# Optimization experiments

Measured on AMD Instinct MI355X. Metric: run time of the kernel, lower is better.

The kernel has to match this reference:

```python
import jax, jax.numpy as jnp
import numpy as np

N = 100000      # nodes
E = 1600000     # edges
G = 64          # graphs in batch
H = 128         # hidden (== num_features)
L = 4           # num_layers
C = 16          # num_classes
NCAND = 100000  # candidate edges
BN_EPS = 1e-5


def setup_inputs() -> dict:
    key = jax.random.key(0)
    ks = jax.random.split(key, 24)
    s = 0.05
    inp = {}
    inp["x"] = jax.random.normal(ks[0], (N, H), dtype=jnp.float32)
    inp["edge_index"] = jax.random.randint(ks[1], (2, E), 0, N)
    inp["batch"] = jnp.sort(jax.random.randint(ks[2], (N,), 0, G))
    inp["candidate_edges"] = jax.random.randint(ks[3], (2, NCAND), 0, N)
    # GIN conv params, stacked over L layers (all layers are H->H since num_features==hidden)
    inp["cW1"] = jax.random.normal(ks[4], (L, H, H), dtype=jnp.float32) * s
    inp["cb1"] = jnp.zeros((L, H), jnp.float32)
    inp["cW2"] = jax.random.normal(ks[5], (L, H, H), dtype=jnp.float32) * s
    inp["cb2"] = jnp.zeros((L, H), jnp.float32)
    inp["cgamma"] = jnp.ones((L, H), jnp.float32)
    inp["cbeta"] = jnp.zeros((L, H), jnp.float32)
    inp["ceps"] = jnp.zeros((L,), jnp.float32)  # train_eps=True, init 0
    # node classifier: L*H -> 2H -> H -> H -> C (dropout is identity in eval)
    inp["ncW1"] = jax.random.normal(ks[6], (L * H, 2 * H), dtype=jnp.float32) * s
    inp["ncb1"] = jnp.zeros((2 * H,), jnp.float32)
    inp["ncW2"] = jax.random.normal(ks[7], (2 * H, H), dtype=jnp.float32) * s
    inp["ncb2"] = jnp.zeros((H,), jnp.float32)
    inp["ncW3"] = jax.random.normal(ks[8], (H, H), dtype=jnp.float32) * s
    inp["ncb3"] = jnp.zeros((H,), jnp.float32)
    inp["ncW4"] = jax.random.normal(ks[9], (H, C), dtype=jnp.float32) * s
    inp["ncb4"] = jnp.zeros((C,), jnp.float32)
    # edge predictor: 2*L*H -> 2H -> H -> 1
    inp["epW1"] = jax.random.normal(ks[10], (2 * L * H, 2 * H), dtype=jnp.float32) * s
    inp["epb1"] = jnp.zeros((2 * H,), jnp.float32)
    inp["epW2"] = jax.random.normal(ks[11], (2 * H, H), dtype=jnp.float32) * s
    inp["epb2"] = jnp.zeros((H,), jnp.float32)
    inp["epW3"] = jax.random.normal(ks[12], (H, 1), dtype=jnp.float32) * s
    inp["epb3"] = jnp.zeros((1,), jnp.float32)
    return inp


def _forward(x, cW1, cb1, cW2, cb2, cgamma, cbeta, ceps,
             ncW1, ncb1, ncW2, ncb2, ncW3, ncb3, ncW4, ncb4,
             epW1, epb1, epW2, epb2, epW3, epb3,
             edge_index, batch, candidate_edges):
    src, dst = edge_index[0], edge_index[1]
    h = x
    xs = []
    for l in range(L):
        # GIN: (1+eps)*x_i + sum_{j->i} x_j  (scatter-add over destination nodes)
        agg = jax.ops.segment_sum(h[src], dst, num_segments=N)
        z = (1.0 + ceps[l]) * h + agg
        z = jax.nn.relu(z @ cW1[l] + cb1[l])
        z = jax.nn.relu(z @ cW2[l] + cb2[l])
        # BatchNorm1d (training-mode batch statistics, biased variance)
        mu = z.mean(axis=0)
        var = jnp.var(z, axis=0)
        h = (z - mu) * jax.lax.rsqrt(var + BN_EPS) * cgamma[l] + cbeta[l]
        xs.append(h)
    emb = jnp.concatenate(xs, axis=-1)  # [N, L*H]
    # global mean pool over graphs
    sums = jax.ops.segment_sum(emb, batch, num_segments=G)
    cnt = jax.ops.segment_sum(jnp.ones((N, 1), emb.dtype), batch, num_segments=G)
    gemb = sums / jnp.maximum(cnt, 1.0)  # [G, L*H]
    t = jax.nn.relu(gemb @ ncW1 + ncb1)
    t = jax.nn.relu(t @ ncW2 + ncb2)
    t = jax.nn.relu(t @ ncW3 + ncb3)
    class_output = jax.nn.log_softmax(t @ ncW4 + ncb4, axis=1)  # [G, C]
    # link prediction: gather node embeddings per candidate edge
    ef = jnp.concatenate([emb[candidate_edges[0]], emb[candidate_edges[1]]], axis=1)  # [NC, 2*L*H]
    u = jax.nn.relu(ef @ epW1 + epb1)
    u = jax.nn.relu(u @ epW2 + epb2)
    edge_scores = jax.nn.sigmoid((u @ epW3 + epb3).squeeze(-1))  # [NC]
    return class_output, edge_scores


def reference(x, cW1, cb1, cW2, cb2, cgamma, cbeta, ceps,
              ncW1, ncb1, ncW2, ncb2, ncW3, ncb3, ncW4, ncb4,
              epW1, epb1, epW2, epb2, epW3, epb3,
              edge_index, batch, candidate_edges):
    return _forward(x, cW1, cb1, cW2, cb2, cgamma, cbeta, ceps,
                    ncW1, ncb1, ncW2, ncb2, ncW3, ncb3, ncW4, ncb4,
                    epW1, epb1, epW2, epb2, epW3, epb3,
                    edge_index, batch, candidate_edges)
```

## Files before the change

kernel.cpp:

```cpp
#include <hip/hip_runtime.h>
#include <math.h>

#define NN 100000
#define EE 1600000
#define GG 64
#define HH 128
#define LL 4
#define CCLS 16
#define NC 100000
#define NB 49
#define LDK 40
#define LDA2 136
#define LDC 260

typedef __attribute__((ext_vector_type(8))) short bf16x8;
typedef __attribute__((ext_vector_type(4))) float f32x4;

__device__ __forceinline__ unsigned short f2bf(float x) {
  union { float f; unsigned int u; } v; v.f = x;
  unsigned int r = v.u + 0x7fffu + ((v.u >> 16) & 1u);
  return (unsigned short)(r >> 16);
}
__device__ __forceinline__ float bl(unsigned u) {
  union { unsigned u; float f; } v; v.u = u << 16; return v.f;
}
__device__ __forceinline__ float bh(unsigned u) {
  union { unsigned u; float f; } v; v.u = u & 0xffff0000u; return v.f;
}

__global__ void hist_kernel(const int* __restrict__ dst, int* __restrict__ cnt, int E) {
  int e = blockIdx.x * 256 + threadIdx.x;
  if (e < E) atomicAdd(&cnt[dst[e]], 1);
}

__global__ __launch_bounds__(256) void scan_p1(const int* __restrict__ cnt,
                                               int* __restrict__ bsum, int n) {
  __shared__ int red[256];
  int tid = threadIdx.x;
  int base = blockIdx.x * 1024 + tid * 4;
  int s = 0;
  if (base + 3 < n) {
    int4 v = *(const int4*)(cnt + base);
    s = v.x + v.y + v.z + v.w;
  } else {
    for (int i = 0; i < 4; ++i) if (base + i < n) s += cnt[base + i];
  }
  red[tid] = s;
  __syncthreads();
  for (int st = 128; st >= 1; st >>= 1) {
    if (tid < st) red[tid] += red[tid + st];
    __syncthreads();
  }
  if (tid == 0) bsum[blockIdx.x] = red[0];
}

__global__ void scan_p2(int* __restrict__ bsum, int* __restrict__ rowptr,
                        int* __restrict__ bcursor, int nb, int n) {
  __shared__ int buf[128];
  int tid = threadIdx.x;
  int v = (tid < nb) ? bsum[tid] : 0;
  buf[tid] = v;
  __syncthreads();
  for (int off = 1; off < 128; off <<= 1) {
    int t = (tid >= off) ? buf[tid - off] : 0;
    __syncthreads();
    buf[tid] += t;
    __syncthreads();
  }
  if (tid < nb) bsum[tid] = buf[tid] - v;
  if (tid == 127) rowptr[n] = buf[127];
  __syncthreads();
  if (tid < NB) bcursor[tid] = bsum[2 * tid];
}

__global__ __launch_bounds__(256) void scan_p3(const int* __restrict__ cnt,
                                               const int* __restrict__ bsum,
                                               int* __restrict__ rowptr,
                                               int* __restrict__ cursor, int n) {
  __shared__ int red[256];
  int tid = threadIdx.x;
  int base = blockIdx.x * 1024 + tid * 4;
  int v[4] = {0, 0, 0, 0};
  if (base + 3 < n) {
    int4 t = *(const int4*)(cnt + base);
    v[0] = t.x; v[1] = t.y; v[2] = t.z; v[3] = t.w;
  } else {
    for (int i = 0; i < 4; ++i) if (base + i < n) v[i] = cnt[base + i];
  }
  int s = v[0] + v[1] + v[2] + v[3];
  red[tid] = s;
  __syncthreads();
  for (int off = 1; off < 256; off <<= 1) {
    int t = (tid >= off) ? red[tid - off] : 0;
    __syncthreads();
    red[tid] += t;
    __syncthreads();
  }
  int run = bsum[blockIdx.x] + red[tid] - s;
  int4 o;
  o.x = run; o.y = run + v[0]; o.z = o.y + v[1]; o.w = o.z + v[2];
  if (base + 3 < n) {
    *(int4*)(rowptr + base) = o;
    *(int4*)(cursor + base) = o;
  } else {
    int oo[4] = {o.x, o.y, o.z, o.w};
    for (int i = 0; i < 4; ++i)
      if (base + i < n) { rowptr[base + i] = oo[i]; cursor[base + i] = oo[i]; }
  }
}

__global__ __launch_bounds__(256) void partition_kernel(const int* __restrict__ src,
                                                        const int* __restrict__ dst,
                                                        int* __restrict__ bcursor,
                                                        int2* __restrict__ pairs, int E) {
  __shared__ int sS[4096];
  __shared__ int sD[4096];
  __shared__ int hist[NB];
  __shared__ int base[NB];
  int tid = threadIdx.x;
  int base_e = blockIdx.x * 4096;
  int cnt = min(4096, E - base_e);
  if (tid < NB) hist[tid] = 0;
  for (int i = tid * 4; i < cnt; i += 1024) {
    if (i + 3 < cnt) {
      *(int4*)(sS + i) = *(const int4*)(src + base_e + i);
      *(int4*)(sD + i) = *(const int4*)(dst + base_e + i);
    } else {
      for (int k = i; k < cnt; ++k) { sS[k] = src[base_e + k]; sD[k] = dst[base_e + k]; }
    }
  }
  __syncthreads();
  for (int i = tid; i < cnt; i += 256) atomicAdd(&hist[sD[i] >> 11], 1);
  __syncthreads();
  if (tid < NB) {
    base[tid] = atomicAdd(&bcursor[tid], hist[tid]);
    hist[tid] = 0;
  }
  __syncthreads();
  for (int i = tid; i < cnt; i += 256) {
    int d = sD[i];
    int b = d >> 11;
    int off = atomicAdd(&hist[b], 1);
    pairs[base[b] + off] = make_int2(sS[i], d);
  }
}

__global__ __launch_bounds__(256) void scatter_csr(const int2* __restrict__ pairs,
                                                   const int* __restrict__ rowptr,
                                                   int* __restrict__ cursor,
                                                   int* __restrict__ csr_src) {
  int b = blockIdx.x % 56;
  int slice = blockIdx.x / 56;
  if (b >= NB) return;
  int start = rowptr[b * 2048];
  int endn = min((b + 1) * 2048, NN);
  int end = rowptr[endn];
  for (int i = start + slice * 256 + threadIdx.x; i < end; i += 8 * 256) {
    int2 p = pairs[i];
    int pos = atomicAdd(&cursor[p.y], 1);
    csr_src[pos] = p.x;
  }
}

#define NF2B (NN * HH / 4)
#define NCVW (LL * 16384 + 262144 + 32768)
__global__ void convert_all(const float* __restrict__ x, unsigned short* __restrict__ x16,
                            const float* __restrict__ cW1, const float* __restrict__ cW2,
                            unsigned short* __restrict__ WT1, unsigned short* __restrict__ WT2,
                            const float* __restrict__ epW1, unsigned short* __restrict__ W1T,
                            const float* __restrict__ epW2, unsigned short* __restrict__ W2T) {
  int gi = blockIdx.x * 256 + threadIdx.x;
  if (gi < NF2B) {
    float4 v = ((const float4*)x)[gi];
    unsigned short r[4] = {f2bf(v.x), f2bf(v.y), f2bf(v.z), f2bf(v.w)};
    *(uint2*)(x16 + (size_t)gi * 4) = *(uint2*)r;
    return;
  }
  int idx = gi - NF2B;
  if (idx < LL * 16384) {
    int l = idx >> 14, r = idx & 16383, k = r >> 7, n = r & 127;
    WT1[l * 16384 + n * 128 + k] = f2bf(cW1[idx]);
    WT2[l * 16384 + n * 128 + k] = f2bf(cW2[idx]);
  } else if (idx < LL * 16384 + 262144) {
    int j = idx - LL * 16384;
    int k = j >> 8, n = j & 255;
    W1T[(size_t)n * 1024 + k] = f2bf(epW1[j]);
  } else if (idx < NCVW) {
    int j = idx - LL * 16384 - 262144;
    int k = j >> 7, n = j & 127;
    W2T[(size_t)n * 256 + k] = f2bf(epW2[j]);
  }
}

__global__ void aggregate_bf16(const unsigned short* __restrict__ h16, int ld,
                               const int* __restrict__ rowptr,
                               const int* __restrict__ csr_src,
                               const float* __restrict__ ceps_l,
                               const float* __restrict__ bnsum_prev,
                               const float* __restrict__ bnsumsq_prev,
                               const float* __restrict__ gamma_prev,
                               const float* __restrict__ beta_prev,
                               unsigned short* __restrict__ out, int n) {
  int wave = threadIdx.x >> 6;
  int lane = threadIdx.x & 63;
  int sub = lane >> 4;
  int li = lane & 15;
  int node = blockIdx.x * 16 + wave * 4 + sub;
  if (node >= n) return;
  int c8 = li * 8;
  float eps1 = 1.0f + *ceps_l;
  float sc[8], off[8];
  if (bnsum_prev) {
    const float inv_n = 1.0f / (float)NN;
#pragma unroll
    for (int k = 0; k < 8; ++k) {
      int c = c8 + k;
      float mu = bnsum_prev[c] * inv_n;
      float var = bnsumsq_prev[c] * inv_n - mu * mu;
      float s = rsqrtf(var + 1e-5f) * gamma_prev[c];
      sc[k] = s;
      off[k] = beta_prev[c] - s * mu;
    }
  } else {
#pragma unroll
    for (int k = 0; k < 8; ++k) { sc[k] = 1.f; off[k] = 0.f; }
  }
  float acc[8] = {};
  int b = rowptr[node], e = rowptr[node + 1];
  int j = b;
  for (; j + 8 <= e; j += 8) {
    uint4 u[8];
#pragma unroll
    for (int t = 0; t < 8; ++t) {
      int s = csr_src[j + t];
      u[t] = *(const uint4*)(h16 + (size_t)s * ld + c8);
    }
#pragma unroll
    for (int t = 0; t < 8; ++t) {
      acc[0] += bl(u[t].x); acc[1] += bh(u[t].x);
      acc[2] += bl(u[t].y); acc[3] += bh(u[t].y);
      acc[4] += bl(u[t].z); acc[5] += bh(u[t].z);
      acc[6] += bl(u[t].w); acc[7] += bh(u[t].w);
    }
  }
  for (; j < e; ++j) {
    int s = csr_src[j];
    uint4 u = *(const uint4*)(h16 + (size_t)s * ld + c8);
    acc[0] += bl(u.x); acc[1] += bh(u.x);
    acc[2] += bl(u.y); acc[3] += bh(u.y);
    acc[4] += bl(u.z); acc[5] += bh(u.z);
    acc[6] += bl(u.w); acc[7] += bh(u.w);
  }
  uint4 hu = *(const uint4*)(h16 + (size_t)node * ld + c8);
  acc[0] = fmaf(eps1, bl(hu.x), acc[0]); acc[1] = fmaf(eps1, bh(hu.x), acc[1]);
  acc[2] = fmaf(eps1, bl(hu.y), acc[2]); acc[3] = fmaf(eps1, bh(hu.y), acc[3]);
  acc[4] = fmaf(eps1, bl(hu.z), acc[4]); acc[5] = fmaf(eps1, bh(hu.z), acc[5]);
  acc[6] = fmaf(eps1, bl(hu.w), acc[6]); acc[7] = fmaf(eps1, bh(hu.w), acc[7]);
  float degw = (float)(e - b) + eps1;
  unsigned short o[8];
#pragma unroll
  for (int i = 0; i < 8; ++i) o[i] = f2bf(fmaf(sc[i], acc[i], degw * off[i]));
  *(uint4*)(out + (size_t)node * 128 + c8) = *(uint4*)o;
}

__global__ __launch_bounds__(256) void trunk_fused(
    const unsigned short* __restrict__ A16,
    const unsigned short* __restrict__ W1T, const float* __restrict__ b1,
    const unsigned short* __restrict__ W2T, const float* __restrict__ b2,
    float* __restrict__ bnsum, float* __restrict__ bnsumsq,
    unsigned short* __restrict__ C16 , int M) {
  __shared__ unsigned short As[128 * LDA2];
  __shared__ unsigned short Bs[128 * LDA2];
  const int tid = threadIdx.x;
  const int bm = blockIdx.x * 128;
  const int lane = tid & 63;
  const int wave = tid >> 6;
  const int wr = (wave >> 1) << 6;
  const int wc = (wave & 1) << 6;
  const int ar = tid >> 1;
  const int ah = (tid & 1) << 4;
  int gra = bm + ar; if (gra >= M) gra = M - 1;
  const unsigned short* Arow = A16 + (size_t)gra * 128;
  const unsigned short* B1row = W1T + (size_t)ar * 128;
  const int mrow = lane & 15;
  const int kq = (lane >> 4) << 3;

  {
    uint4 aR[8], bR[8];
#pragma unroll
    for (int i = 0; i < 4; ++i) {
      aR[2 * i]     = *(const uint4*)(Arow + (i << 5) + ah);
      aR[2 * i + 1] = *(const uint4*)(Arow + (i << 5) + ah + 8);
      bR[2 * i]     = *(const uint4*)(B1row + (i << 5) + ah);
      bR[2 * i + 1] = *(const uint4*)(B1row + (i << 5) + ah + 8);
    }
#pragma unroll
    for (int i = 0; i < 4; ++i) {
      *(uint4*)(As + ar * LDA2 + (i << 5) + ah)     = aR[2 * i];
      *(uint4*)(As + ar * LDA2 + (i << 5) + ah + 8) = aR[2 * i + 1];
      *(uint4*)(Bs + ar * LDA2 + (i << 5) + ah)     = bR[2 * i];
      *(uint4*)(Bs + ar * LDA2 + (i << 5) + ah + 8) = bR[2 * i + 1];
    }
  }
  f32x4 acc[4][4] = {};
  __syncthreads();
#pragma unroll
  for (int ks = 0; ks < 4; ++ks) {
    const int k0 = ks << 5;
    bf16x8 af[4], bfv[4];
#pragma unroll
    for (int t = 0; t < 4; ++t)
      af[t] = *(const bf16x8*)(As + (wr + t * 16 + mrow) * LDA2 + k0 + kq);
#pragma unroll
    for (int t = 0; t < 4; ++t)
      bfv[t] = *(const bf16x8*)(Bs + (wc + t * 16 + mrow) * LDA2 + k0 + kq);
#pragma unroll
    for (int mt = 0; mt < 4; ++mt)
#pragma unroll
      for (int nt = 0; nt < 4; ++nt)
        acc[mt][nt] = __builtin_amdgcn_mfma_f32_16x16x32_bf16(af[mt], bfv[nt], acc[mt][nt], 0, 0, 0);
  }
  uint4 w2[8];
  {
    const unsigned short* B2row = W2T + (size_t)ar * 128;
#pragma unroll
    for (int i = 0; i < 4; ++i) {
      w2[2 * i]     = *(const uint4*)(B2row + (i << 5) + ah);
      w2[2 * i + 1] = *(const uint4*)(B2row + (i << 5) + ah + 8);
    }
  }
  __syncthreads();
  const int crow = (lane >> 4) << 2;
  const int ccol = lane & 15;
#pragma unroll
  for (int nt = 0; nt < 4; ++nt) {
    int c = wc + nt * 16 + ccol;
    float bz = b1[c];
#pragma unroll
    for (int mt = 0; mt < 4; ++mt) {
      int rl = wr + mt * 16 + crow;
#pragma unroll
      for (int i = 0; i < 4; ++i)
        As[(rl + i) * LDA2 + c] = f2bf(fmaxf(acc[mt][nt][i] + bz, 0.f));
    }
  }
#pragma unroll
  for (int i = 0; i < 4; ++i) {
    *(uint4*)(Bs + ar * LDA2 + (i << 5) + ah)     = w2[2 * i];
    *(uint4*)(Bs + ar * LDA2 + (i << 5) + ah + 8) = w2[2 * i + 1];
  }
#pragma unroll
  for (int mt = 0; mt < 4; ++mt)
#pragma unroll
    for (int nt = 0; nt < 4; ++nt)
      acc[mt][nt] = (f32x4){0.f, 0.f, 0.f, 0.f};
  __syncthreads();
#pragma unroll
  for (int ks = 0; ks < 4; ++ks) {
    const int k0 = ks << 5;
    bf16x8 af[4], bfv[4];
#pragma unroll
    for (int t = 0; t < 4; ++t)
      af[t] = *(const bf16x8*)(As + (wr + t * 16 + mrow) * LDA2 + k0 + kq);
#pragma unroll
    for (int t = 0; t < 4; ++t)
      bfv[t] = *(const bf16x8*)(Bs + (wc + t * 16 + mrow) * LDA2 + k0 + kq);
#pragma unroll
    for (int mt = 0; mt < 4; ++mt)
#pragma unroll
      for (int nt = 0; nt < 4; ++nt)
        acc[mt][nt] = __builtin_amdgcn_mfma_f32_16x16x32_bf16(af[mt], bfv[nt], acc[mt][nt], 0, 0, 0);
  }
  __syncthreads();
#pragma unroll
  for (int nt = 0; nt < 4; ++nt) {
    int c = wc + nt * 16 + ccol;
    float bz = b2[c];
    float s = 0.f, q = 0.f;
#pragma unroll
    for (int mt = 0; mt < 4; ++mt) {
      int rl = wr + mt * 16 + crow;
      int rbase = bm + rl;
#pragma unroll
      for (int i = 0; i < 4; ++i) {
        float v = fmaxf(acc[mt][nt][i] + bz, 0.f);
        Bs[(rl + i) * LDA2 + c] = f2bf(v);
        if (rbase + i < M) { s += v; q += v * v; }
      }
    }
    s += __shfl_xor(s, 16, 64);
    s += __shfl_xor(s, 32, 64);
    q += __shfl_xor(q, 16, 64);
    q += __shfl_xor(q, 32, 64);
    if (lane < 16) {
      atomicAdd(&bnsum[c], s);
      atomicAdd(&bnsumsq[c], q);
    }
  }
  __syncthreads();
#pragma unroll
  for (int p = 0; p < 8; ++p) {
    int r = p * 16 + (tid >> 4);
    int q8 = (tid & 15) * 8;
    if (bm + r < M)
      *(uint4*)(C16 + (size_t)(bm + r) * 512 + q8) =
          *(const uint4*)(Bs + r * LDA2 + q8);
  }
}

__global__ void bn_all(unsigned short* __restrict__ z ,
                       const float* __restrict__ sum, const float* __restrict__ sumsq,
                       const float* __restrict__ gamma, const float* __restrict__ beta) {
  int idx = blockIdx.x * 256 + threadIdx.x;
  if (idx >= NN * 64) return;
  int r = idx >> 6, c8 = (idx & 63) << 3;
  uint4 v = *(const uint4*)(z + (size_t)r * 512 + c8);
  float f[8] = {bl(v.x), bh(v.x), bl(v.y), bh(v.y), bl(v.z), bh(v.z), bl(v.w), bh(v.w)};
  const float inv_n = 1.0f / (float)NN;
  unsigned short o[8];
#pragma unroll
  for (int j = 0; j < 8; ++j) {
    int c = c8 + j;
    float mu = sum[c] * inv_n;
    float var = sumsq[c] * inv_n - mu * mu;
    float scv = rsqrtf(var + 1e-5f) * gamma[c];
    o[j] = f2bf((f[j] - mu) * scv + beta[c]);
  }
  *(uint4*)(z + (size_t)r * 512 + c8) = *(uint4*)o;
}

__global__ __launch_bounds__(512, 4) void ep_fused(
    const unsigned short* __restrict__ emb16, const int* __restrict__ cand,
    const unsigned short* __restrict__ W1T ,
    const float* __restrict__ b1,
    const unsigned short* __restrict__ W2T ,
    const float* __restrict__ b2, const float* __restrict__ epW3,
    const float* __restrict__ epb3,
    float* __restrict__ out, int M) {
  __shared__ unsigned short smem[128 * LDC];
  __shared__ float sDotA[128];
  __shared__ float sDotB[128];
  unsigned short* const As0 = smem;
  unsigned short* const As1 = smem + 128 * LDK;
  unsigned short* const Bs0 = smem + 2 * 128 * LDK;
  unsigned short* const Bs1 = smem + 2 * 128 * LDK + 256 * LDK;
  const int tid = threadIdx.x;
  const int bm = blockIdx.x * 128;
  const int lane = tid & 63;
  const int wave = tid >> 6;
  const int wr = (wave >> 2) << 6;
  const int wc = (wave & 3) << 6;
  f32x4 acc[4][4] = {};
  const int ar = tid >> 2;
  const int ah = (tid & 3) << 3;
  int gra = bm + ar; if (gra >= M) gra = M - 1;
  const int node0 = cand[gra];
  const int node1 = cand[NC + gra];
  const int br = tid >> 1;
  const int bh8 = (tid & 1) << 4;
  const unsigned short* Brow = W1T + (size_t)br * 1024 + bh8;
  const unsigned short* Arow0 = emb16 + (size_t)node0 * 512 + ah;
  const unsigned short* Arow1 = emb16 + (size_t)node1 * 512 + ah - 512;
  const int mrow = lane & 15;
  const int kq = (lane >> 4) << 3;

  auto ldA = [&](int k) -> uint4 {
    const unsigned short* p = (k < 16) ? Arow0 : Arow1;
    return *(const uint4*)(p + (k << 5));
  };
  auto ldB0v = [&](int k) -> uint4 { return *(const uint4*)(Brow + (k << 5)); };
  auto ldB1v = [&](int k) -> uint4 { return *(const uint4*)(Brow + (k << 5) + 8); };
  auto stTile = [&](unsigned short* Ab, unsigned short* Bb, uint4 a, uint4 x0, uint4 x1) {
    *(uint4*)(Ab + ar * LDK + ah) = a;
    *(uint4*)(Bb + br * LDK + bh8) = x0;
    *(uint4*)(Bb + br * LDK + bh8 + 8) = x1;
  };
  auto mma_step = [&](const unsigned short* A, const unsigned short* B) {
    bf16x8 af[4], bfv[4];
#pragma unroll
    for (int t = 0; t < 4; ++t)
      af[t] = *(const bf16x8*)(A + (wr + t * 16 + mrow) * LDK + kq);
#pragma unroll
    for (int t = 0; t < 4; ++t)
      bfv[t] = *(const bf16x8*)(B + (wc + t * 16 + mrow) * LDK + kq);
#pragma unroll
    for (int mt = 0; mt < 4; ++mt)
#pragma unroll
      for (int nt = 0; nt < 4; ++nt)
        acc[mt][nt] = __builtin_amdgcn_mfma_f32_16x16x32_bf16(af[mt], bfv[nt], acc[mt][nt], 0, 0, 0);
  };

  uint4 aA, aB, b0, b1v;
  {
    uint4 a0 = ldA(0), x0 = ldB0v(0), x1 = ldB1v(0);
    stTile(As0, Bs0, a0, x0, x1);
    aA = ldA(1); b0 = ldB0v(1); b1v = ldB1v(1);
    aB = ldA(2);
  }
  __syncthreads();
  for (int it = 0; it < 16; ++it) {
    const int s0 = 2 * it;
    stTile(As1, Bs1, aA, b0, b1v);
    if (s0 + 3 < 32) aA = ldA(s0 + 3);
    if (s0 + 2 < 32) { b0 = ldB0v(s0 + 2); b1v = ldB1v(s0 + 2); }
    mma_step(As0, Bs0);
    __syncthreads();
    const int s1 = s0 + 1;
    if (s1 < 31) {
      stTile(As0, Bs0, aB, b0, b1v);
      if (s1 + 3 < 32) aB = ldA(s1 + 3);
      if (s1 + 2 < 32) { b0 = ldB0v(s1 + 2); b1v = ldB1v(s1 + 2); }
    }
    mma_step(As1, Bs1);
    __syncthreads();
  }

  const int crow = (lane >> 4) << 2;
  const int ccol = lane & 15;
#pragma unroll
  for (int nt = 0; nt < 4; ++nt) {
    int c = wc + nt * 16 + ccol;
    float bz = b1[c];
#pragma unroll
    for (int mt = 0; mt < 4; ++mt) {
      int rl = wr + mt * 16 + crow;
#pragma unroll
      for (int i = 0; i < 4; ++i)
        smem[(rl + i) * LDC + c] = f2bf(fmaxf(acc[mt][nt][i] + bz, 0.f));
    }
  }
  __syncthreads();
  const int wr2 = (wave >> 1) << 5;
  const int wc2 = (wave & 1) << 6;
  f32x4 acc2[2][4] = {};
  for (int ks = 0; ks < 8; ++ks) {
    const int k0 = ks << 5;
    bf16x8 af[2], bfv[4];
#pragma unroll
    for (int t = 0; t < 2; ++t)
      af[t] = *(const bf16x8*)(smem + (wr2 + t * 16 + mrow) * LDC + k0 + kq);
#pragma unroll
    for (int t = 0; t < 4; ++t)
      bfv[t] = *(const bf16x8*)(W2T + (size_t)(wc2 + t * 16 + mrow) * 256 + k0 + kq);
#pragma unroll
    for (int mt = 0; mt < 2; ++mt)
#pragma unroll
      for (int nt = 0; nt < 4; ++nt)
        acc2[mt][nt] = __builtin_amdgcn_mfma_f32_16x16x32_bf16(af[mt], bfv[nt], acc2[mt][nt], 0, 0, 0);
  }
  float w3v[4], bz2[4];
#pragma unroll
  for (int nt = 0; nt < 4; ++nt) {
    int c = wc2 + nt * 16 + ccol;
    w3v[nt] = epW3[c];
    bz2[nt] = b2[c];
  }
  float* sBank = (wave & 1) ? sDotB : sDotA;
#pragma unroll
  for (int mt = 0; mt < 2; ++mt) {
#pragma unroll
    for (int i = 0; i < 4; ++i) {
      int rl = wr2 + mt * 16 + crow + i;
      float p = 0.f;
#pragma unroll
      for (int nt = 0; nt < 4; ++nt)
        p = fmaf(fmaxf(acc2[mt][nt][i] + bz2[nt], 0.f), w3v[nt], p);
      p += __shfl_xor(p, 1, 64);
      p += __shfl_xor(p, 2, 64);
      p += __shfl_xor(p, 4, 64);
      p += __shfl_xor(p, 8, 64);
      if ((lane & 15) == 0) sBank[rl] = p;
    }
  }
  __syncthreads();
  if (tid < 128) {
    int r = bm + tid;
    if (r < M) out[r] = 1.f / (1.f + expf(-(sDotA[tid] + sDotB[tid] + epb3[0])));
  }
}

__global__ __launch_bounds__(256) void pool_bf16(const unsigned short* __restrict__ emb16,
                                                 const int* __restrict__ batch,
                                                 float* __restrict__ gsum) {
  __shared__ int se[2];
  __shared__ float sRed[512];
  int g = blockIdx.x;
  int chunk = blockIdx.y;
  int tid = threadIdx.x;
  if (tid < 2) {
    int x = g + tid;
    int lo = 0, hi = NN;
    while (lo < hi) {
      int mid = (lo + hi) >> 1;
      if (batch[mid] < x) lo = mid + 1; else hi = mid;
    }
    se[tid] = lo;
  }
  __syncthreads();
  int s = se[0], e = se[1];
  int len = e - s;
  int per = (len + 7) >> 3;
  int r0 = s + chunk * per;
  int r1 = min(r0 + per, e);
  int c8 = (tid & 63) * 8;
  int wgrp = tid >> 6;
  float acc[8] = {};
  for (int r = r0 + wgrp; r < r1; r += 4) {
    uint4 u = *(const uint4*)(emb16 + (size_t)r * 512 + c8);
    acc[0] += bl(u.x); acc[1] += bh(u.x);
    acc[2] += bl(u.y); acc[3] += bh(u.y);
    acc[4] += bl(u.z); acc[5] += bh(u.z);
    acc[6] += bl(u.w); acc[7] += bh(u.w);
  }
  if (wgrp == 0) {
#pragma unroll
    for (int j = 0; j < 8; ++j) sRed[c8 + j] = acc[j];
  }
  __syncthreads();
  for (int w = 1; w < 4; ++w) {
    if (wgrp == w) {
#pragma unroll
      for (int j = 0; j < 8; ++j) sRed[c8 + j] += acc[j];
    }
    __syncthreads();
  }
  if (r0 < r1 && tid < 128) {
#pragma unroll
    for (int j = 0; j < 4; ++j)
      atomicAdd(&gsum[g * 512 + tid * 4 + j], sRed[tid * 4 + j]);
  }
}

__global__ __launch_bounds__(256) void nc_fused(
    const float* __restrict__ gsum, const int* __restrict__ batch,
    const float* __restrict__ W1, const float* __restrict__ b1,
    const float* __restrict__ W2, const float* __restrict__ b2,
    const float* __restrict__ W3, const float* __restrict__ b3,
    const float* __restrict__ W4, const float* __restrict__ b4,
    float* __restrict__ out) {
  __shared__ float row[512];
  __shared__ float t1[256];
  __shared__ float t2[128];
  __shared__ float t3s[128];
  __shared__ float lg[16];
  __shared__ int se[2];
  int g = blockIdx.x;
  int tid = threadIdx.x;
  if (tid < 2) {
    int x = g + tid;
    int lo = 0, hi = NN;
    while (lo < hi) {
      int mid = (lo + hi) >> 1;
      if (batch[mid] < x) lo = mid + 1; else hi = mid;
    }
    se[tid] = lo;
  }
  __syncthreads();
  float inv = 1.0f / fmaxf((float)(se[1] - se[0]), 1.0f);
  row[tid] = gsum[g * 512 + tid] * inv;
  row[tid + 256] = gsum[g * 512 + tid + 256] * inv;
  __syncthreads();
  {
    float acc = b1[tid];
#pragma unroll 8
    for (int k = 0; k < 512; ++k) acc = fmaf(row[k], W1[k * 256 + tid], acc);
    t1[tid] = fmaxf(acc, 0.f);
  }
  __syncthreads();
  if (tid < 128) {
    float acc = b2[tid];
#pragma unroll 8
    for (int k = 0; k < 256; ++k) acc = fmaf(t1[k], W2[k * 128 + tid], acc);
    t2[tid] = fmaxf(acc, 0.f);
  }
  __syncthreads();
  if (tid < 128) {
    float acc = b3[tid];
#pragma unroll 8
    for (int k = 0; k < 128; ++k) acc = fmaf(t2[k], W3[k * 128 + tid], acc);
    t3s[tid] = fmaxf(acc, 0.f);
  }
  __syncthreads();
  if (tid < 16) {
    float acc = b4[tid];
#pragma unroll 8
    for (int k = 0; k < 128; ++k) acc = fmaf(t3s[k], W4[k * 16 + tid], acc);
    lg[tid] = acc;
  }
  __syncthreads();
  if (tid < 16) {
    float v = lg[tid];
    float m = v;
    for (int j = 0; j < 16; ++j) m = fmaxf(m, lg[j]);
    float s = 0.f;
    for (int j = 0; j < 16; ++j) s += expf(lg[j] - m);
    out[g * 16 + tid] = v - m - logf(s);
  }
}

extern "C" void kernel_launch(void* const* d_in, const int* in_sizes, int n_in,
                              void* d_out, int out_size, void* d_ws, size_t ws_size,
                              hipStream_t stream) {
  const float* x = (const float*)d_in[0];
  const int* edge_index = (const int*)d_in[1];
  const int* batch = (const int*)d_in[2];
  const int* cand = (const int*)d_in[3];
  const float* cW1 = (const float*)d_in[4];
  const float* cb1 = (const float*)d_in[5];
  const float* cW2 = (const float*)d_in[6];
  const float* cb2 = (const float*)d_in[7];
  const float* cgamma = (const float*)d_in[8];
  const float* cbeta = (const float*)d_in[9];
  const float* ceps = (const float*)d_in[10];
  const float* ncW1 = (const float*)d_in[11];
  const float* ncb1 = (const float*)d_in[12];
  const float* ncW2 = (const float*)d_in[13];
  const float* ncb2 = (const float*)d_in[14];
  const float* ncW3 = (const float*)d_in[15];
  const float* ncb3 = (const float*)d_in[16];
  const float* ncW4 = (const float*)d_in[17];
  const float* ncb4 = (const float*)d_in[18];
  const float* epW1 = (const float*)d_in[19];
  const float* epb1 = (const float*)d_in[20];
  const float* epW2 = (const float*)d_in[21];
  const float* epb2 = (const float*)d_in[22];
  const float* epW3 = (const float*)d_in[23];
  const float* epb3 = (const float*)d_in[24];

  char* ws = (char*)d_ws;
  size_t off = 0;
  auto alloc = [&](size_t bytes) -> void* {
    off = (off + 255) & ~(size_t)255;
    void* p = ws + off;
    off += bytes;
    return p;
  };
  size_t zz_bytes = (size_t)NN * 4 + 512 * 4 + 512 * 4 + (size_t)GG * 512 * 4;
  char* zz = (char*)alloc(zz_bytes);
  int* cnt = (int*)zz;
  float* bnsum = (float*)(zz + (size_t)NN * 4);
  float* bnsumsq = bnsum + 512;
  float* gsum = bnsumsq + 512;
  int* rowptr = (int*)alloc((size_t)(NN + 1) * 4);
  int* cursor = (int*)alloc((size_t)NN * 4);
  int* csr_src = (int*)alloc((size_t)EE * 4);
  int2* pairs = (int2*)alloc((size_t)EE * 8);
  int* bsum = (int*)alloc(128 * 4);
  int* bcursor = (int*)alloc(64 * 4);
  unsigned short* x16 = (unsigned short*)alloc((size_t)NN * 128 * 2);
  unsigned short* g16a = (unsigned short*)alloc((size_t)NN * 128 * 2);
  unsigned short* emb16 = (unsigned short*)alloc((size_t)NN * 512 * 2);
  unsigned short* WT1 = (unsigned short*)alloc((size_t)LL * 16384 * 2);
  unsigned short* WT2 = (unsigned short*)alloc((size_t)LL * 16384 * 2);
  unsigned short* W1T = (unsigned short*)alloc((size_t)1024 * 256 * 2);
  unsigned short* W2T = (unsigned short*)alloc((size_t)256 * 128 * 2);

  const int* esrc = edge_index;
  const int* edst = edge_index + EE;
  const int nblk = (NN + 1023) / 1024;
  const int nech = (EE + 4095) / 4096;

  hipMemsetAsync(zz, 0, zz_bytes, stream);
  hist_kernel<<<(EE + 255) / 256, 256, 0, stream>>>(edst, cnt, EE);
  scan_p1<<<nblk, 256, 0, stream>>>(cnt, bsum, NN);
  scan_p2<<<1, 128, 0, stream>>>(bsum, rowptr, bcursor, nblk, NN);
  scan_p3<<<nblk, 256, 0, stream>>>(cnt, bsum, rowptr, cursor, NN);
  partition_kernel<<<nech, 256, 0, stream>>>(esrc, edst, bcursor, pairs, EE);
  scatter_csr<<<56 * 8, 256, 0, stream>>>(pairs, rowptr, cursor, csr_src);
  convert_all<<<(NF2B + NCVW + 255) / 256, 256, 0, stream>>>(
      x, x16, cW1, cW2, WT1, WT2, epW1, W1T, epW2, W2T);

  for (int l = 0; l < LL; ++l) {
    const unsigned short* h16 = (l == 0) ? x16 : (emb16 + (size_t)(l - 1) * 128);
    int ld = (l == 0) ? 128 : 512;
    aggregate_bf16<<<(NN + 15) / 16, 256, 0, stream>>>(
        h16, ld, rowptr, csr_src, ceps + l,
        (l == 0) ? nullptr : bnsum + (l - 1) * 128,
        (l == 0) ? nullptr : bnsumsq + (l - 1) * 128,
        (l == 0) ? nullptr : cgamma + (l - 1) * 128,
        (l == 0) ? nullptr : cbeta + (l - 1) * 128,
        g16a, NN);
    trunk_fused<<<(NN + 127) / 128, 256, 0, stream>>>(
        g16a, WT1 + (size_t)l * 16384, cb1 + l * 128,
        WT2 + (size_t)l * 16384, cb2 + l * 128,
        bnsum + l * 128, bnsumsq + l * 128, emb16 + (size_t)l * 128, NN);
  }
  bn_all<<<(NN * 64 + 255) / 256, 256, 0, stream>>>(emb16, bnsum, bnsumsq, cgamma, cbeta);

  pool_bf16<<<dim3(GG, 8), 256, 0, stream>>>(emb16, batch, gsum);
  nc_fused<<<GG, 256, 0, stream>>>(gsum, batch, ncW1, ncb1, ncW2, ncb2, ncW3, ncb3,
                                   ncW4, ncb4, (float*)d_out);

  ep_fused<<<(NC + 127) / 128, 512, 0, stream>>>(
      emb16, cand, W1T, epb1, W2T, epb2, epW3, epb3,
      (float*)d_out + GG * CCLS, NC);
}
```

Before: 1.027 ms.

## Fold final BatchNorm affine into edge-predictor weights and pooled class input

Removes the separate pass that normalized the full node-embedding matrix in place. The per-channel BN scale is folded into the bf16 transposed epW1, and the shift is folded into a new per-output bias computed by a small prep kernel. The node-classifier applies the affine to pooled means instead, relying on linearity of mean pooling. This saves a full read-write of the 100000x512 embedding buffer, at the cost of slightly different bf16 rounding since scaled weights are quantized instead of normalized activations.

New measurement: 999.4 us. -2.7%, faster.

```diff
diff --git a/kernel.cpp b/kernel.cpp
--- a/kernel.cpp
+++ b/kernel.cpp
@@ -163,11 +163,10 @@
 }
 
 #define NF2B (NN * HH / 4)
-#define NCVW (LL * 16384 + 262144 + 32768)
+#define NCVW (LL * 16384 + 32768)
 __global__ void convert_all(const float* __restrict__ x, unsigned short* __restrict__ x16,
                             const float* __restrict__ cW1, const float* __restrict__ cW2,
                             unsigned short* __restrict__ WT1, unsigned short* __restrict__ WT2,
-                            const float* __restrict__ epW1, unsigned short* __restrict__ W1T,
                             const float* __restrict__ epW2, unsigned short* __restrict__ W2T) {
   int gi = blockIdx.x * 256 + threadIdx.x;
   if (gi < NF2B) {
@@ -181,15 +180,45 @@
     int l = idx >> 14, r = idx & 16383, k = r >> 7, n = r & 127;
     WT1[l * 16384 + n * 128 + k] = f2bf(cW1[idx]);
     WT2[l * 16384 + n * 128 + k] = f2bf(cW2[idx]);
-  } else if (idx < LL * 16384 + 262144) {
+  } else if (idx < NCVW) {
     int j = idx - LL * 16384;
-    int k = j >> 8, n = j & 255;
-    W1T[(size_t)n * 1024 + k] = f2bf(epW1[j]);
-  } else if (idx < NCVW) {
-    int j = idx - LL * 16384 - 262144;
     int k = j >> 7, n = j & 127;
     W2T[(size_t)n * 256 + k] = f2bf(epW2[j]);
   }
+}
+
+__global__ __launch_bounds__(256) void ep_w1_prep(
+    const float* __restrict__ epW1, const float* __restrict__ epb1,
+    const float* __restrict__ bnsum, const float* __restrict__ bnsumsq,
+    const float* __restrict__ gamma, const float* __restrict__ beta,
+    unsigned short* __restrict__ W1T, float* __restrict__ b1x) {
+  __shared__ float red[256];
+  int n = blockIdx.x;
+  int tid = threadIdx.x;
+  const float inv_n = 1.0f / (float)NN;
+  int k0 = tid * 4;
+  unsigned short w16[4];
+  float part = 0.f;
+#pragma unroll
+  for (int j = 0; j < 4; ++j) {
+    int k = k0 + j;
+    int c = k & 511;
+    float mu = bnsum[c] * inv_n;
+    float var = bnsumsq[c] * inv_n - mu * mu;
+    float s = rsqrtf(var + 1e-5f) * gamma[c];
+    float o = beta[c] - s * mu;
+    float w = epW1[(size_t)k * 256 + n];
+    w16[j] = f2bf(s * w);
+    part += o * w;
+  }
+  *(uint2*)(W1T + (size_t)n * 1024 + k0) = *(uint2*)w16;
+  red[tid] = part;
+  __syncthreads();
+  for (int st = 128; st >= 1; st >>= 1) {
+    if (tid < st) red[tid] += red[tid + st];
+    __syncthreads();
+  }
+  if (tid == 0) b1x[n] = epb1[n] + red[0];
 }
 
 __global__ void aggregate_bf16(const unsigned short* __restrict__ h16, int ld,
@@ -406,27 +435,6 @@
       *(uint4*)(C16 + (size_t)(bm + r) * 512 + q8) =
           *(const uint4*)(Bs + r * LDA2 + q8);
   }
-}
-
-__global__ void bn_all(unsigned short* __restrict__ z ,
-                       const float* __restrict__ sum, const float* __restrict__ sumsq,
-                       const float* __restrict__ gamma, const float* __restrict__ beta) {
-  int idx = blockIdx.x * 256 + threadIdx.x;
-  if (idx >= NN * 64) return;
-  int r = idx >> 6, c8 = (idx & 63) << 3;
-  uint4 v = *(const uint4*)(z + (size_t)r * 512 + c8);
-  float f[8] = {bl(v.x), bh(v.x), bl(v.y), bh(v.y), bl(v.z), bh(v.z), bl(v.w), bh(v.w)};
-  const float inv_n = 1.0f / (float)NN;
-  unsigned short o[8];
-#pragma unroll
-  for (int j = 0; j < 8; ++j) {
-    int c = c8 + j;
-    float mu = sum[c] * inv_n;
-    float var = sumsq[c] * inv_n - mu * mu;
-    float scv = rsqrtf(var + 1e-5f) * gamma[c];
-    o[j] = f2bf((f[j] - mu) * scv + beta[c]);
-  }
-  *(uint4*)(z + (size_t)r * 512 + c8) = *(uint4*)o;
 }
 
 __global__ __launch_bounds__(512, 4) void ep_fused(
@@ -633,6 +641,8 @@
 
 __global__ __launch_bounds__(256) void nc_fused(
     const float* __restrict__ gsum, const int* __restrict__ batch,
+    const float* __restrict__ bnsum, const float* __restrict__ bnsumsq,
+    const float* __restrict__ gamma, const float* __restrict__ beta,
     const float* __restrict__ W1, const float* __restrict__ b1,
     const float* __restrict__ W2, const float* __restrict__ b2,
     const float* __restrict__ W3, const float* __restrict__ b3,
@@ -657,8 +667,16 @@
   }
   __syncthreads();
   float inv = 1.0f / fmaxf((float)(se[1] - se[0]), 1.0f);
-  row[tid] = gsum[g * 512 + tid] * inv;
-  row[tid + 256] = gsum[g * 512 + tid + 256] * inv;
+  const float inv_n = 1.0f / (float)NN;
+#pragma unroll
+  for (int h = 0; h < 2; ++h) {
+    int c = tid + h * 256;
+    float mu = bnsum[c] * inv_n;
+    float var = bnsumsq[c] * inv_n - mu * mu;
+    float s = rsqrtf(var + 1e-5f) * gamma[c];
+    float o = beta[c] - s * mu;
+    row[c] = fmaf(gsum[g * 512 + c] * inv, s, o);
+  }
   __syncthreads();
   {
     float acc = b1[tid];
@@ -754,6 +772,7 @@
   unsigned short* WT2 = (unsigned short*)alloc((size_t)LL * 16384 * 2);
   unsigned short* W1T = (unsigned short*)alloc((size_t)1024 * 256 * 2);
   unsigned short* W2T = (unsigned short*)alloc((size_t)256 * 128 * 2);
+  float* b1x = (float*)alloc(256 * 4);
 
   const int* esrc = edge_index;
   const int* edst = edge_index + EE;
@@ -768,7 +787,7 @@
   partition_kernel<<<nech, 256, 0, stream>>>(esrc, edst, bcursor, pairs, EE);
   scatter_csr<<<56 * 8, 256, 0, stream>>>(pairs, rowptr, cursor, csr_src);
   convert_all<<<(NF2B + NCVW + 255) / 256, 256, 0, stream>>>(
-      x, x16, cW1, cW2, WT1, WT2, epW1, W1T, epW2, W2T);
+      x, x16, cW1, cW2, WT1, WT2, epW2, W2T);
 
   for (int l = 0; l < LL; ++l) {
     const unsigned short* h16 = (l == 0) ? x16 : (emb16 + (size_t)(l - 1) * 128);
@@ -785,13 +804,15 @@
         WT2 + (size_t)l * 16384, cb2 + l * 128,
         bnsum + l * 128, bnsumsq + l * 128, emb16 + (size_t)l * 128, NN);
   }
-  bn_all<<<(NN * 64 + 255) / 256, 256, 0, stream>>>(emb16, bnsum, bnsumsq, cgamma, cbeta);
+  ep_w1_prep<<<256, 256, 0, stream>>>(epW1, epb1, bnsum, bnsumsq, cgamma, cbeta,
+                                      W1T, b1x);
 
   pool_bf16<<<dim3(GG, 8), 256, 0, stream>>>(emb16, batch, gsum);
-  nc_fused<<<GG, 256, 0, stream>>>(gsum, batch, ncW1, ncb1, ncW2, ncb2, ncW3, ncb3,
+  nc_fused<<<GG, 256, 0, stream>>>(gsum, batch, bnsum, bnsumsq, cgamma, cbeta,
+                                   ncW1, ncb1, ncW2, ncb2, ncW3, ncb3,
                                    ncW4, ncb4, (float*)d_out);
 
   ep_fused<<<(NC + 127) / 128, 512, 0, stream>>>(
-      emb16, cand, W1T, epb1, W2T, epb2, epW3, epb3,
+      emb16, cand, W1T, b1x, W2T, epb2, epW3, epb3,
       (float*)d_out + GG * CCLS, NC);
 }
```
